# Optimization experiments

Measured on AMD Instinct MI355X. Metric: run time of the kernel, lower is better.

Reference implementation:

```python
import jax, jax.numpy as jnp
import numpy as np

N_NODES = 50000
N_EDGES = 800000
IN_FEATS = 128
OUT_FEATS = 128


def setup_inputs() -> dict:
    key = jax.random.key(0)
    k_feat, k_src, k_dst, k_w1, k_w2, k_lw = jax.random.split(key, 6)
    feat = jax.random.normal(k_feat, (N_NODES, IN_FEATS), dtype=jnp.float32)
    src_idx = jax.random.randint(k_src, (N_EDGES,), 0, N_NODES, dtype=jnp.int64 if jax.config.jax_enable_x64 else jnp.int32)
    dst_idx = jax.random.randint(k_dst, (N_EDGES,), 0, N_NODES, dtype=jnp.int64 if jax.config.jax_enable_x64 else jnp.int32)
    # xavier-uniform-ish scales
    w1_lim = float(np.sqrt(6.0 / (2 * IN_FEATS + IN_FEATS)))
    w2_lim = float(np.sqrt(6.0 / (IN_FEATS + OUT_FEATS)))
    lw_lim = float(np.sqrt(2.0) * np.sqrt(6.0 / (IN_FEATS + OUT_FEATS)))
    weight1 = jax.random.uniform(k_w1, (2 * IN_FEATS, IN_FEATS), jnp.float32, -w1_lim, w1_lim)
    weight2 = jax.random.uniform(k_w2, (IN_FEATS, OUT_FEATS), jnp.float32, -w2_lim, w2_lim)
    loop_weight = jax.random.uniform(k_lw, (IN_FEATS, OUT_FEATS), jnp.float32, -lw_lim, lw_lim)
    bias = jnp.zeros((OUT_FEATS,), dtype=jnp.float32)
    return {
        "feat": feat,
        "src_idx": src_idx,
        "dst_idx": dst_idx,
        "weight1": weight1,
        "weight2": weight2,
        "loop_weight": loop_weight,
        "bias": bias,
    }


def reference(feat, src_idx, dst_idx, weight1, weight2, loop_weight, bias):
    # Gather per-edge src/dst features and concat: [E, 2*d]
    feat_msg = jnp.concatenate([feat[src_idx], feat[dst_idx]], axis=-1)
    # 2-layer edge MLP: relu(msg @ W1) @ W2 -> [E, out]
    e_msg = jnp.matmul(jax.nn.relu(jnp.matmul(feat_msg, weight1)), weight2)
    # Scatter-sum to destination nodes: [N, out]
    rst = jax.ops.segment_sum(e_msg, dst_idx, num_segments=feat.shape[0])
    # bias + residual loop message
    rst = rst + bias + jnp.matmul(feat, loop_weight)
    return rst
```

## Files before the change

kernel.cpp:

```cpp
#include <hip/hip_runtime.h>

typedef __attribute__((ext_vector_type(8))) unsigned short ushort8v;
typedef __attribute__((ext_vector_type(8))) short short8v;
typedef __attribute__((ext_vector_type(4))) float f32x4;

#define CAP 64
#define BINSTRIDE 2560

__device__ inline unsigned short f2bf(float f) {
    union { float f; unsigned u; } v; v.f = f;
    unsigned u = v.u;
    unsigned r = (u + 0x7FFFu + ((u >> 16) & 1u)) >> 16;
    return (unsigned short)r;
}
__device__ inline float bf2f(unsigned short h) {
    union { unsigned u; float f; } v; v.u = ((unsigned)h) << 16;
    return v.f;
}
__device__ inline unsigned pkbf(float lo, float hi) {
    unsigned r;
    asm("v_cvt_pk_bf16_f32 %0, %1, %2" : "=v"(r) : "v"(lo), "v"(hi));
    return r;
}

__global__ __launch_bounds__(256) void prep_weights(
    const float* __restrict__ W1, const float* __restrict__ W2,
    const float* __restrict__ LW,
    unsigned short* __restrict__ W1t, unsigned short* __restrict__ W3t,
    int* __restrict__ binCur, int NBINS) {
    int tid = threadIdx.x;
    if (blockIdx.x == 0)
        for (int j = tid; j < NBINS; j += 256) binCur[j] = 0;
    int i = blockIdx.x * 256 + tid;
    if (i < 32768) {
        int jj = i >> 7, k = i & 127;
        float v = (jj < 128) ? W1[k * 128 + jj] : W1[(128 + k) * 128 + (jj - 128)];
        W1t[i] = f2bf(v);
    } else {
        int i2 = i - 32768;
        int n = i2 >> 8, k = i2 & 255;
        float v = (k < 128) ? W2[k * 128 + n] : LW[(k - 128) * 128 + n];
        W3t[i2] = f2bf(v);
    }
}

__global__ __launch_bounds__(256) void gemm1_bin(
    const float* __restrict__ feat, const unsigned short* __restrict__ W1t,
    unsigned short* __restrict__ AB,
    const int* __restrict__ src, const int* __restrict__ dst,
    int* __restrict__ binCur, unsigned* __restrict__ binPairs,
    int E, int NC, int NT, int M, int NBINS) {
    __shared__ unsigned short smem[(128 + 256) * 64];
    const int tid = threadIdx.x;
    const int bid = blockIdx.x;

    if ((bid & 1) == 0) {
        int tile = bid >> 1;
        if (tile >= NT) return;
        int m0 = tile * 128;
        const int lane = tid & 63, w = tid >> 6;
        const int wr = w >> 1, wc = w & 1;
        const int q = lane >> 4, ln = lane & 15;
        unsigned short* As = smem;
        unsigned short* Bs = smem + 128 * 64;

        f32x4 acc[4][8];
#pragma unroll
        for (int i = 0; i < 4; i++)
#pragma unroll
            for (int j = 0; j < 8; j++) acc[i][j] = (f32x4)0.f;

        for (int kk = 0; kk < 128; kk += 64) {
#pragma unroll
            for (int i = 0; i < 4; i++) {
                int id = i * 256 + tid;
                int r = id >> 3, bb = id & 7, gr = m0 + r;
                unsigned short* dstp = As + r * 64 + ((bb ^ (r & 7)) * 8);
                float4 lo = make_float4(0.f, 0.f, 0.f, 0.f), hi = lo;
                if (gr < M) {
                    const float* p = feat + (size_t)gr * 128 + kk + bb * 8;
                    lo = *(const float4*)p;
                    hi = *(const float4*)(p + 4);
                }
                *(uint4*)dstp = make_uint4(pkbf(lo.x, lo.y), pkbf(lo.z, lo.w),
                                           pkbf(hi.x, hi.y), pkbf(hi.z, hi.w));
            }
#pragma unroll
            for (int i = 0; i < 8; i++) {
                int id = i * 256 + tid;
                int r = id >> 3, bb = id & 7;
                ushort8v v = *(const ushort8v*)(W1t + (size_t)r * 128 + kk + bb * 8);
                *(ushort8v*)(Bs + r * 64 + ((bb ^ (r & 7)) * 8)) = v;
            }
            __syncthreads();
#pragma unroll
            for (int ks = 0; ks < 2; ks++) {
                short8v af[4], bv[8];
#pragma unroll
                for (int ti = 0; ti < 4; ti++) {
                    int m = wr * 64 + ti * 16 + ln;
                    int blk = (ks * 4 + q) ^ (m & 7);
                    af[ti] = *(const short8v*)(As + m * 64 + blk * 8);
                }
#pragma unroll
                for (int tj = 0; tj < 8; tj++) {
                    int n = wc * 128 + tj * 16 + ln;
                    int blk = (ks * 4 + q) ^ (n & 7);
                    bv[tj] = *(const short8v*)(Bs + n * 64 + blk * 8);
                }
#pragma unroll
                for (int ti = 0; ti < 4; ti++)
#pragma unroll
                    for (int tj = 0; tj < 8; tj++)
                        acc[ti][tj] = __builtin_amdgcn_mfma_f32_16x16x32_bf16(
                            af[ti], bv[tj], acc[ti][tj], 0, 0, 0);
            }
            if (kk == 0) __syncthreads();
        }
#pragma unroll
        for (int ti = 0; ti < 4; ti++) {
            int rowb = m0 + wr * 64 + ti * 16 + q * 4;
#pragma unroll
            for (int tj = 0; tj < 8; tj++) {
                int col = wc * 128 + tj * 16 + ln;
                f32x4 c = acc[ti][tj];
#pragma unroll
                for (int r = 0; r < 4; r++) {
                    int row = rowb + r;
                    if (row < M)
                        AB[(size_t)row * 256 + col] = f2bf(c[r]);
                }
            }
        }
    } else {
        int chunk = bid >> 1;
        if (chunk >= NC) return;
        int* hist = (int*)smem;
        int* bse = hist + 512;
        for (int j = tid; j < NBINS; j += 256) hist[j] = 0;

        int s[8], d[8];
        int base = chunk * 2048 + tid * 8;
        if (base + 7 < E) {
            int4 s0 = *(const int4*)(src + base);
            int4 s1 = *(const int4*)(src + base + 4);
            int4 d0 = *(const int4*)(dst + base);
            int4 d1 = *(const int4*)(dst + base + 4);
            s[0] = s0.x; s[1] = s0.y; s[2] = s0.z; s[3] = s0.w;
            s[4] = s1.x; s[5] = s1.y; s[6] = s1.z; s[7] = s1.w;
            d[0] = d0.x; d[1] = d0.y; d[2] = d0.z; d[3] = d0.w;
            d[4] = d1.x; d[5] = d1.y; d[6] = d1.z; d[7] = d1.w;
        } else {
#pragma unroll
            for (int k = 0; k < 8; k++) {
                int ee = base + k;
                if (ee < E) { d[k] = dst[ee]; s[k] = src[ee]; }
                else d[k] = -1;
            }
        }
        __syncthreads();
#pragma unroll
        for (int k = 0; k < 8; k++)
            if (d[k] >= 0) atomicAdd(&hist[d[k] >> 7], 1);
        __syncthreads();
        for (int j = tid; j < NBINS; j += 256) {
            int c = hist[j];
            bse[j] = c ? atomicAdd(&binCur[j], c) : 0;
            hist[j] = 0;
        }
        __syncthreads();
#pragma unroll
        for (int k = 0; k < 8; k++) {
            if (d[k] < 0) continue;
            int b = d[k] >> 7;
            int p = bse[b] + atomicAdd(&hist[b], 1);
            if (p < BINSTRIDE)
                binPairs[(size_t)b * BINSTRIDE + p] =
                    ((unsigned)(d[k] & 127) << 16) | (unsigned)s[k];
        }
    }
}

__global__ __launch_bounds__(256) void build_buckets(
    const int* __restrict__ binCur, const unsigned* __restrict__ binPairs,
    int* __restrict__ cur, unsigned short* __restrict__ eSrc,
    int N, int NBINS) {
    __shared__ unsigned pairs[BINSTRIDE];
    __shared__ int deg[128], rnk[128];
    int b = blockIdx.x, tid = threadIdx.x;
    if (b >= NBINS) return;
    int cnt = min(binCur[b], BINSTRIDE);
    if (tid < 128) { deg[tid] = 0; rnk[tid] = 0; }
    __syncthreads();
    for (int i = tid; i < cnt; i += 256) {
        unsigned pr = binPairs[(size_t)b * BINSTRIDE + i];
        pairs[i] = pr;
        atomicAdd(&deg[pr >> 16], 1);
    }
    __syncthreads();
    int node0 = b << 7;
    if (tid < 128 && node0 + tid < N) cur[node0 + tid] = deg[tid];
    for (int i = tid; i < cnt; i += 256) {
        unsigned pr = pairs[i];
        int dl = pr >> 16;
        int pos = atomicAdd(&rnk[dl], 1);
        if (pos < CAP)
            eSrc[(size_t)(node0 + dl) * CAP + pos] = (unsigned short)(pr & 0xFFFF);
    }
}

template <int BK, int AMODE, bool OUT_BF16>
__device__ void gemm_tile(
    unsigned short* As, unsigned short* Bs,
    const unsigned short* __restrict__ Abf, int lda,
    const float* __restrict__ Af32,
    const unsigned short* __restrict__ Bt, int ldb, int nRowsB,
    void* __restrict__ Cout, int ldc,
    const float* __restrict__ bias, int M, int K, int m0, int n0) {
    const int tid = threadIdx.x;
    const int lane = tid & 63;
    const int w = tid >> 6;
    const int wr = w >> 1, wc = w & 1;
    const int q = lane >> 4, ln = lane & 15;
    const int BPR = BK / 8;
    const int ITERS = BK / 16;

    f32x4 acc[4][4];
#pragma unroll
    for (int i = 0; i < 4; i++)
#pragma unroll
        for (int j = 0; j < 4; j++) acc[i][j] = (f32x4)0.f;

    for (int kk = 0; kk < K; kk += BK) {
        const bool aF32 = (AMODE == 1) || (AMODE == 2 && kk >= 128);
#pragma unroll
        for (int i = 0; i < ITERS; i++) {
            int id = i * 256 + tid;
            int r = id / BPR, bb = id % BPR;
            int gr = m0 + r;
            unsigned short* dstp = As + r * BK + ((bb ^ (r & (BPR - 1))) * 8);
            if (aF32) {
                float4 lo = make_float4(0.f, 0.f, 0.f, 0.f), hi = lo;
                if (gr < M) {
                    const float* p = Af32 + (size_t)gr * 128 +
                                     (AMODE == 2 ? kk - 128 : kk) + bb * 8;
                    lo = *(const float4*)p;
                    hi = *(const float4*)(p + 4);
                }
                *(uint4*)dstp = make_uint4(pkbf(lo.x, lo.y), pkbf(lo.z, lo.w),
                                           pkbf(hi.x, hi.y), pkbf(hi.z, hi.w));
            } else {
                ushort8v v = (ushort8v)(unsigned short)0;
                if (gr < M) v = *(const ushort8v*)(Abf + (size_t)gr * lda + kk + bb * 8);
                *(ushort8v*)dstp = v;
            }
        }
#pragma unroll
        for (int i = 0; i < ITERS; i++) {
            int id = i * 256 + tid;
            int r = id / BPR, bb = id % BPR;
            ushort8v v = (ushort8v)(unsigned short)0;
            int gr = n0 + r;
            if (gr < nRowsB) v = *(const ushort8v*)(Bt + (size_t)gr * ldb + kk + bb * 8);
            *(ushort8v*)(Bs + r * BK + ((bb ^ (r & (BPR - 1))) * 8)) = v;
        }
        __syncthreads();
#pragma unroll
        for (int ks = 0; ks < BK / 32; ks++) {
            short8v af[4], bfv[4];
#pragma unroll
            for (int ti = 0; ti < 4; ti++) {
                int m = wr * 64 + ti * 16 + ln;
                int blk = (ks * 4 + q) ^ (m & (BPR - 1));
                af[ti] = *(const short8v*)(As + m * BK + blk * 8);
            }
#pragma unroll
            for (int tj = 0; tj < 4; tj++) {
                int n = wc * 64 + tj * 16 + ln;
                int blk = (ks * 4 + q) ^ (n & (BPR - 1));
                bfv[tj] = *(const short8v*)(Bs + n * BK + blk * 8);
            }
#pragma unroll
            for (int ti = 0; ti < 4; ti++)
#pragma unroll
                for (int tj = 0; tj < 4; tj++)
                    acc[ti][tj] = __builtin_amdgcn_mfma_f32_16x16x32_bf16(
                        af[ti], bfv[tj], acc[ti][tj], 0, 0, 0);
        }
        if (kk + BK < K) __syncthreads();
    }

#pragma unroll
    for (int ti = 0; ti < 4; ti++) {
        int rowb = m0 + wr * 64 + ti * 16 + q * 4;
#pragma unroll
        for (int tj = 0; tj < 4; tj++) {
            int col = n0 + wc * 64 + tj * 16 + ln;
            f32x4 c = acc[ti][tj];
            float bv = 0.f;
            if (!OUT_BF16 && bias) bv = bias[col];
#pragma unroll
            for (int r = 0; r < 4; r++) {
                int row = rowb + r;
                if (row < M) {
                    if (OUT_BF16)
                        ((unsigned short*)Cout)[(size_t)row * ldc + col] = f2bf(c[r]);
                    else
                        ((float*)Cout)[(size_t)row * ldc + col] = c[r] + bv;
                }
            }
        }
    }
}

__global__ __launch_bounds__(256) void gemm2_kernel(
    const unsigned short* __restrict__ S2, const float* __restrict__ feat,
    const unsigned short* __restrict__ W3t,
    float* __restrict__ out, const float* __restrict__ bias, int M) {
    __shared__ unsigned short smem[2 * 128 * 64];
    gemm_tile<64, 2, false>(smem, smem + 128 * 64, S2, 128, feat, W3t, 256, 128,
                            (void*)out, 128, bias, M, 256, blockIdx.x * 128, 0);
}

__global__ __launch_bounds__(256) void gather_kernel(
    const unsigned short* __restrict__ AB, const int* __restrict__ cur,
    const unsigned short* __restrict__ eSrc,
    unsigned short* __restrict__ S2, int N) {
    int wid = (blockIdx.x * 256 + threadIdx.x) >> 6;
    int lane = threadIdx.x & 63;
    if (wid >= N) return;
    int num = min(cur[wid], CAP);
    size_t start = (size_t)wid * CAP;
    int half = lane >> 5, ln32 = lane & 31;
    ushort4 bv = *(const ushort4*)(AB + (size_t)wid * 256 + 128 + ln32 * 4);
    float b0 = bf2f(bv.x), b1 = bf2f(bv.y), b2 = bf2f(bv.z), b3 = bf2f(bv.w);
    float p0 = 0.f, p1 = 0.f, p2 = 0.f, p3 = 0.f;

    int mySrc = (lane < num) ? (int)eSrc[start + lane] : 0;
    int j = 0;
    for (; j + 16 <= num; j += 16) {
        ushort4 v[8];
#pragma unroll
        for (int u = 0; u < 8; u++) {
            int s = __shfl(mySrc, j + 2 * u + half);
            v[u] = *(const ushort4*)(AB + (size_t)s * 256 + ln32 * 4);
        }
#pragma unroll
        for (int u = 0; u < 8; u++) {
            p0 += fmaxf(bf2f(v[u].x) + b0, 0.f);
            p1 += fmaxf(bf2f(v[u].y) + b1, 0.f);
            p2 += fmaxf(bf2f(v[u].z) + b2, 0.f);
            p3 += fmaxf(bf2f(v[u].w) + b3, 0.f);
        }
    }
    for (; j + 4 <= num; j += 4) {
        ushort4 v[2];
#pragma unroll
        for (int u = 0; u < 2; u++) {
            int s = __shfl(mySrc, j + 2 * u + half);
            v[u] = *(const ushort4*)(AB + (size_t)s * 256 + ln32 * 4);
        }
#pragma unroll
        for (int u = 0; u < 2; u++) {
            p0 += fmaxf(bf2f(v[u].x) + b0, 0.f);
            p1 += fmaxf(bf2f(v[u].y) + b1, 0.f);
            p2 += fmaxf(bf2f(v[u].z) + b2, 0.f);
            p3 += fmaxf(bf2f(v[u].w) + b3, 0.f);
        }
    }
    for (; j < num; j += 2) {
        int idx = j + half;
        int s = __shfl(mySrc, idx);
        bool ok = idx < num;
        ushort4 v = *(const ushort4*)(AB + (size_t)s * 256 + ln32 * 4);
        float m = ok ? 1.f : 0.f;
        p0 += m * fmaxf(bf2f(v.x) + b0, 0.f);
        p1 += m * fmaxf(bf2f(v.y) + b1, 0.f);
        p2 += m * fmaxf(bf2f(v.z) + b2, 0.f);
        p3 += m * fmaxf(bf2f(v.w) + b3, 0.f);
    }
    p0 += __shfl_xor(p0, 32);
    p1 += __shfl_xor(p1, 32);
    p2 += __shfl_xor(p2, 32);
    p3 += __shfl_xor(p3, 32);
    if (half == 0) {
        *(ushort4*)(S2 + (size_t)wid * 128 + ln32 * 4) =
            make_ushort4(f2bf(p0), f2bf(p1), f2bf(p2), f2bf(p3));
    }
}

extern "C" void kernel_launch(void* const* d_in, const int* in_sizes, int n_in,
                              void* d_out, int out_size, void* d_ws, size_t ws_size,
                              hipStream_t stream) {
    const float* feat = (const float*)d_in[0];
    const int* src = (const int*)d_in[1];
    const int* dst = (const int*)d_in[2];
    const float* W1 = (const float*)d_in[3];
    const float* W2 = (const float*)d_in[4];
    const float* LW = (const float*)d_in[5];
    const float* bias = (const float*)d_in[6];
    float* out = (float*)d_out;

    const int N = in_sizes[0] / 128;
    const int E = in_sizes[1];
    const int NBINS = (N + 127) / 128;

    char* ws = (char*)d_ws;
    unsigned short* S2 = (unsigned short*)ws;
    size_t off = (size_t)N * 128 * 2;
    unsigned short* AB = (unsigned short*)(ws + off);
    off += (size_t)N * 256 * 2;
    unsigned short* W1t = (unsigned short*)(ws + off);
    off += (size_t)256 * 128 * 2;
    unsigned short* W3t = (unsigned short*)(ws + off);
    off += (size_t)128 * 256 * 2;
    int* cur = (int*)(ws + off);
    off += (size_t)N * 4;
    unsigned short* eSrc = (unsigned short*)(ws + off);
    off += (size_t)N * CAP * 2;
    int* binCur = (int*)(ws + off);
    off += (size_t)NBINS * 4;
    unsigned* binPairs = (unsigned*)(ws + off);
    off += (size_t)NBINS * BINSTRIDE * 4;

    prep_weights<<<256, 256, 0, stream>>>(W1, W2, LW, W1t, W3t, binCur, NBINS);

    int NT = (N + 127) / 128;
    int NC = (E + 2047) / 2048;
    int mx = NT > NC ? NT : NC;
    gemm1_bin<<<2 * mx, 256, 0, stream>>>(
        feat, W1t, AB, src, dst, binCur, binPairs, E, NC, NT, N, NBINS);

    build_buckets<<<NBINS, 256, 0, stream>>>(binCur, binPairs, cur, eSrc, N, NBINS);

    gather_kernel<<<(N + 3) / 4, 256, 0, stream>>>(AB, cur, eSrc, S2, N);

    gemm2_kernel<<<(N + 127) / 128, 256, 0, stream>>>(S2, feat, W3t, out, bias, N);
}
```

Measured before the change: 182.1 us.

## Fuse gather into gemm2 via LDS staging and split gemm1 into N-halves

The per-node gather-reduce now runs inside the second GEMM kernel. Each block aggregates 128 nodes into a swizzled LDS A-tile, then multiplies by the combined W2/loop weights, so the S2 intermediate no longer makes a round trip through global memory and one launch is dropped. gemm1 now computes 128x128 output tiles instead of 128x256, which halves its accumulator registers and LDS footprint and improves occupancy. Binning chunks grow to 4096 edges, and gemm and binning blocks are interleaved 4:1. The risk is that the fused kernel has only about 391 blocks, each doing a long serial gather with heavy 64KB LDS use, so latency hiding may suffer relative to the previous wave-per-node gather.

```diff
diff --git a/kernel.cpp b/kernel.cpp
--- a/kernel.cpp
+++ b/kernel.cpp
@@ -49,26 +49,27 @@
     unsigned short* __restrict__ AB,
     const int* __restrict__ src, const int* __restrict__ dst,
     int* __restrict__ binCur, unsigned* __restrict__ binPairs,
-    int E, int NC, int NT, int M, int NBINS) {
-    __shared__ unsigned short smem[(128 + 256) * 64];
+    int E, int NC, int NT2, int M, int NBINS) {
+    __shared__ unsigned short smem[2 * 128 * 64];
     const int tid = threadIdx.x;
     const int bid = blockIdx.x;
-
-    if ((bid & 1) == 0) {
-        int tile = bid >> 1;
-        if (tile >= NT) return;
-        int m0 = tile * 128;
+    const int r5 = bid % 5;
+
+    if (r5 < 4) {
+        int g = (bid / 5) * 4 + r5;
+        if (g >= NT2) return;
+        int m0 = (g >> 1) * 128, n0 = (g & 1) * 128;
         const int lane = tid & 63, w = tid >> 6;
         const int wr = w >> 1, wc = w & 1;
         const int q = lane >> 4, ln = lane & 15;
         unsigned short* As = smem;
         unsigned short* Bs = smem + 128 * 64;
 
-        f32x4 acc[4][8];
+        f32x4 acc[4][4];
 #pragma unroll
         for (int i = 0; i < 4; i++)
 #pragma unroll
-            for (int j = 0; j < 8; j++) acc[i][j] = (f32x4)0.f;
+            for (int j = 0; j < 4; j++) acc[i][j] = (f32x4)0.f;
 
         for (int kk = 0; kk < 128; kk += 64) {
 #pragma unroll
@@ -86,16 +87,16 @@
                                            pkbf(hi.x, hi.y), pkbf(hi.z, hi.w));
             }
 #pragma unroll
-            for (int i = 0; i < 8; i++) {
+            for (int i = 0; i < 4; i++) {
                 int id = i * 256 + tid;
                 int r = id >> 3, bb = id & 7;
-                ushort8v v = *(const ushort8v*)(W1t + (size_t)r * 128 + kk + bb * 8);
+                ushort8v v = *(const ushort8v*)(W1t + (size_t)(n0 + r) * 128 + kk + bb * 8);
                 *(ushort8v*)(Bs + r * 64 + ((bb ^ (r & 7)) * 8)) = v;
             }
             __syncthreads();
 #pragma unroll
             for (int ks = 0; ks < 2; ks++) {
-                short8v af[4], bv[8];
+                short8v af[4], bv[4];
 #pragma unroll
                 for (int ti = 0; ti < 4; ti++) {
                     int m = wr * 64 + ti * 16 + ln;
@@ -103,15 +104,15 @@
                     af[ti] = *(const short8v*)(As + m * 64 + blk * 8);
                 }
 #pragma unroll
-                for (int tj = 0; tj < 8; tj++) {
-                    int n = wc * 128 + tj * 16 + ln;
+                for (int tj = 0; tj < 4; tj++) {
+                    int n = wc * 64 + tj * 16 + ln;
                     int blk = (ks * 4 + q) ^ (n & 7);
                     bv[tj] = *(const short8v*)(Bs + n * 64 + blk * 8);
                 }
 #pragma unroll
                 for (int ti = 0; ti < 4; ti++)
 #pragma unroll
-                    for (int tj = 0; tj < 8; tj++)
+                    for (int tj = 0; tj < 4; tj++)
                         acc[ti][tj] = __builtin_amdgcn_mfma_f32_16x16x32_bf16(
                             af[ti], bv[tj], acc[ti][tj], 0, 0, 0);
             }
@@ -121,8 +122,8 @@
         for (int ti = 0; ti < 4; ti++) {
             int rowb = m0 + wr * 64 + ti * 16 + q * 4;
 #pragma unroll
-            for (int tj = 0; tj < 8; tj++) {
-                int col = wc * 128 + tj * 16 + ln;
+            for (int tj = 0; tj < 4; tj++) {
+                int col = n0 + wc * 64 + tj * 16 + ln;
                 f32x4 c = acc[ti][tj];
 #pragma unroll
                 for (int r = 0; r < 4; r++) {
@@ -133,34 +134,36 @@
             }
         }
     } else {
-        int chunk = bid >> 1;
+        int chunk = bid / 5;
         if (chunk >= NC) return;
         int* hist = (int*)smem;
         int* bse = hist + 512;
         for (int j = tid; j < NBINS; j += 256) hist[j] = 0;
 
-        int s[8], d[8];
-        int base = chunk * 2048 + tid * 8;
-        if (base + 7 < E) {
-            int4 s0 = *(const int4*)(src + base);
-            int4 s1 = *(const int4*)(src + base + 4);
-            int4 d0 = *(const int4*)(dst + base);
-            int4 d1 = *(const int4*)(dst + base + 4);
-            s[0] = s0.x; s[1] = s0.y; s[2] = s0.z; s[3] = s0.w;
-            s[4] = s1.x; s[5] = s1.y; s[6] = s1.z; s[7] = s1.w;
-            d[0] = d0.x; d[1] = d0.y; d[2] = d0.z; d[3] = d0.w;
-            d[4] = d1.x; d[5] = d1.y; d[6] = d1.z; d[7] = d1.w;
-        } else {
-#pragma unroll
-            for (int k = 0; k < 8; k++) {
-                int ee = base + k;
-                if (ee < E) { d[k] = dst[ee]; s[k] = src[ee]; }
-                else d[k] = -1;
+        int s[16], d[16];
+        int base = chunk * 4096;
+#pragma unroll
+        for (int i = 0; i < 4; i++) {
+            int e = base + i * 1024 + tid * 4;
+            if (e + 3 < E) {
+                int4 dv = *(const int4*)(dst + e);
+                int4 sv = *(const int4*)(src + e);
+                d[i * 4 + 0] = dv.x; d[i * 4 + 1] = dv.y;
+                d[i * 4 + 2] = dv.z; d[i * 4 + 3] = dv.w;
+                s[i * 4 + 0] = sv.x; s[i * 4 + 1] = sv.y;
+                s[i * 4 + 2] = sv.z; s[i * 4 + 3] = sv.w;
+            } else {
+#pragma unroll
+                for (int k = 0; k < 4; k++) {
+                    int ee = e + k;
+                    if (ee < E) { d[i * 4 + k] = dst[ee]; s[i * 4 + k] = src[ee]; }
+                    else d[i * 4 + k] = -1;
+                }
             }
         }
         __syncthreads();
 #pragma unroll
-        for (int k = 0; k < 8; k++)
+        for (int k = 0; k < 16; k++)
             if (d[k] >= 0) atomicAdd(&hist[d[k] >> 7], 1);
         __syncthreads();
         for (int j = tid; j < NBINS; j += 256) {
@@ -170,7 +173,7 @@
         }
         __syncthreads();
 #pragma unroll
-        for (int k = 0; k < 8; k++) {
+        for (int k = 0; k < 16; k++) {
             if (d[k] < 0) continue;
             int b = d[k] >> 7;
             int p = bse[b] + atomicAdd(&hist[b], 1);
@@ -209,85 +212,141 @@
     }
 }
 
-template <int BK, int AMODE, bool OUT_BF16>
-__device__ void gemm_tile(
-    unsigned short* As, unsigned short* Bs,
-    const unsigned short* __restrict__ Abf, int lda,
-    const float* __restrict__ Af32,
-    const unsigned short* __restrict__ Bt, int ldb, int nRowsB,
-    void* __restrict__ Cout, int ldc,
-    const float* __restrict__ bias, int M, int K, int m0, int n0) {
+__global__ __launch_bounds__(256) void gather_gemm2(
+    const unsigned short* __restrict__ AB, const int* __restrict__ cur,
+    const unsigned short* __restrict__ eSrc,
+    const float* __restrict__ feat, const unsigned short* __restrict__ W3t,
+    float* __restrict__ out, const float* __restrict__ bias, int M) {
+    __shared__ unsigned short As[128 * 128];
+    __shared__ unsigned short Bs[128 * 128];
     const int tid = threadIdx.x;
-    const int lane = tid & 63;
-    const int w = tid >> 6;
+    const int lane = tid & 63, w = tid >> 6;
+    const int m0 = blockIdx.x * 128;
+    const int half = lane >> 5, ln32 = lane & 31;
+
+    for (int i = 0; i < 32; i++) {
+        int r = w * 32 + i;
+        int wid = m0 + r;
+        int num = (wid < M) ? min(cur[wid], CAP) : 0;
+        size_t start = (size_t)wid * CAP;
+        float b0 = 0.f, b1 = 0.f, b2 = 0.f, b3 = 0.f;
+        if (wid < M) {
+            ushort4 bv = *(const ushort4*)(AB + (size_t)wid * 256 + 128 + ln32 * 4);
+            b0 = bf2f(bv.x); b1 = bf2f(bv.y); b2 = bf2f(bv.z); b3 = bf2f(bv.w);
+        }
+        float p0 = 0.f, p1 = 0.f, p2 = 0.f, p3 = 0.f;
+        int mySrc = (lane < num) ? (int)eSrc[start + lane] : 0;
+        int j = 0;
+        for (; j + 16 <= num; j += 16) {
+            ushort4 v[8];
+#pragma unroll
+            for (int u = 0; u < 8; u++) {
+                int s = __shfl(mySrc, j + 2 * u + half);
+                v[u] = *(const ushort4*)(AB + (size_t)s * 256 + ln32 * 4);
+            }
+#pragma unroll
+            for (int u = 0; u < 8; u++) {
+                p0 += fmaxf(bf2f(v[u].x) + b0, 0.f);
+                p1 += fmaxf(bf2f(v[u].y) + b1, 0.f);
+                p2 += fmaxf(bf2f(v[u].z) + b2, 0.f);
+                p3 += fmaxf(bf2f(v[u].w) + b3, 0.f);
+            }
+        }
+        for (; j + 4 <= num; j += 4) {
+            ushort4 v[2];
+#pragma unroll
+            for (int u = 0; u < 2; u++) {
+                int s = __shfl(mySrc, j + 2 * u + half);
+                v[u] = *(const ushort4*)(AB + (size_t)s * 256 + ln32 * 4);
+            }
+#pragma unroll
+            for (int u = 0; u < 2; u++) {
+                p0 += fmaxf(bf2f(v[u].x) + b0, 0.f);
+                p1 += fmaxf(bf2f(v[u].y) + b1, 0.f);
+                p2 += fmaxf(bf2f(v[u].z) + b2, 0.f);
+                p3 += fmaxf(bf2f(v[u].w) + b3, 0.f);
+            }
+        }
+        for (; j < num; j += 2) {
+            int idx = j + half;
+            int s = __shfl(mySrc, idx);
+            bool ok = idx < num;
+            ushort4 v = *(const ushort4*)(AB + (size_t)s * 256 + ln32 * 4);
+            float m = ok ? 1.f : 0.f;
+            p0 += m * fmaxf(bf2f(v.x) + b0, 0.f);
+            p1 += m * fmaxf(bf2f(v.y) + b1, 0.f);
+            p2 += m * fmaxf(bf2f(v.z) + b2, 0.f);
+            p3 += m * fmaxf(bf2f(v.w) + b3, 0.f);
+        }
+        p0 += __shfl_xor(p0, 32);
+        p1 += __shfl_xor(p1, 32);
+        p2 += __shfl_xor(p2, 32);
+        p3 += __shfl_xor(p3, 32);
+        if (half == 0) {
+            int bb = ln32 >> 1;
+            int off = ((bb ^ (r & 15)) * 8) + (ln32 & 1) * 4;
+            *(ushort4*)(As + r * 128 + off) =
+                make_ushort4(f2bf(p0), f2bf(p1), f2bf(p2), f2bf(p3));
+        }
+    }
+
     const int wr = w >> 1, wc = w & 1;
     const int q = lane >> 4, ln = lane & 15;
-    const int BPR = BK / 8;
-    const int ITERS = BK / 16;
-
     f32x4 acc[4][4];
 #pragma unroll
     for (int i = 0; i < 4; i++)
 #pragma unroll
         for (int j = 0; j < 4; j++) acc[i][j] = (f32x4)0.f;
 
-    for (int kk = 0; kk < K; kk += BK) {
-        const bool aF32 = (AMODE == 1) || (AMODE == 2 && kk >= 128);
-#pragma unroll
-        for (int i = 0; i < ITERS; i++) {
-            int id = i * 256 + tid;
-            int r = id / BPR, bb = id % BPR;
-            int gr = m0 + r;
-            unsigned short* dstp = As + r * BK + ((bb ^ (r & (BPR - 1))) * 8);
-            if (aF32) {
+#pragma unroll
+    for (int step = 0; step < 2; step++) {
+        if (step == 1) {
+#pragma unroll
+            for (int i = 0; i < 8; i++) {
+                int id = i * 256 + tid;
+                int r = id >> 4, bb = id & 15, gr = m0 + r;
+                unsigned short* dstp = As + r * 128 + ((bb ^ (r & 15)) * 8);
                 float4 lo = make_float4(0.f, 0.f, 0.f, 0.f), hi = lo;
                 if (gr < M) {
-                    const float* p = Af32 + (size_t)gr * 128 +
-                                     (AMODE == 2 ? kk - 128 : kk) + bb * 8;
+                    const float* p = feat + (size_t)gr * 128 + bb * 8;
                     lo = *(const float4*)p;
                     hi = *(const float4*)(p + 4);
                 }
                 *(uint4*)dstp = make_uint4(pkbf(lo.x, lo.y), pkbf(lo.z, lo.w),
                                            pkbf(hi.x, hi.y), pkbf(hi.z, hi.w));
-            } else {
-                ushort8v v = (ushort8v)(unsigned short)0;
-                if (gr < M) v = *(const ushort8v*)(Abf + (size_t)gr * lda + kk + bb * 8);
-                *(ushort8v*)dstp = v;
-            }
-        }
-#pragma unroll
-        for (int i = 0; i < ITERS; i++) {
+            }
+        }
+#pragma unroll
+        for (int i = 0; i < 8; i++) {
             int id = i * 256 + tid;
-            int r = id / BPR, bb = id % BPR;
-            ushort8v v = (ushort8v)(unsigned short)0;
-            int gr = n0 + r;
-            if (gr < nRowsB) v = *(const ushort8v*)(Bt + (size_t)gr * ldb + kk + bb * 8);
-            *(ushort8v*)(Bs + r * BK + ((bb ^ (r & (BPR - 1))) * 8)) = v;
+            int r = id >> 4, bb = id & 15;
+            ushort8v v = *(const ushort8v*)(W3t + (size_t)r * 256 + step * 128 + bb * 8);
+            *(ushort8v*)(Bs + r * 128 + ((bb ^ (r & 15)) * 8)) = v;
         }
         __syncthreads();
 #pragma unroll
-        for (int ks = 0; ks < BK / 32; ks++) {
-            short8v af[4], bfv[4];
+        for (int ks = 0; ks < 4; ks++) {
+            short8v af[4], bv[4];
 #pragma unroll
             for (int ti = 0; ti < 4; ti++) {
                 int m = wr * 64 + ti * 16 + ln;
-                int blk = (ks * 4 + q) ^ (m & (BPR - 1));
-                af[ti] = *(const short8v*)(As + m * BK + blk * 8);
+                int blk = (ks * 4 + q) ^ (m & 15);
+                af[ti] = *(const short8v*)(As + m * 128 + blk * 8);
             }
 #pragma unroll
             for (int tj = 0; tj < 4; tj++) {
                 int n = wc * 64 + tj * 16 + ln;
-                int blk = (ks * 4 + q) ^ (n & (BPR - 1));
-                bfv[tj] = *(const short8v*)(Bs + n * BK + blk * 8);
+                int blk = (ks * 4 + q) ^ (n & 15);
+                bv[tj] = *(const short8v*)(Bs + n * 128 + blk * 8);
             }
 #pragma unroll
             for (int ti = 0; ti < 4; ti++)
 #pragma unroll
                 for (int tj = 0; tj < 4; tj++)
                     acc[ti][tj] = __builtin_amdgcn_mfma_f32_16x16x32_bf16(
-                        af[ti], bfv[tj], acc[ti][tj], 0, 0, 0);
-        }
-        if (kk + BK < K) __syncthreads();
+                        af[ti], bv[tj], acc[ti][tj], 0, 0, 0);
+        }
+        if (step == 0) __syncthreads();
     }
 
 #pragma unroll
@@ -295,97 +354,16 @@
         int rowb = m0 + wr * 64 + ti * 16 + q * 4;
 #pragma unroll
         for (int tj = 0; tj < 4; tj++) {
-            int col = n0 + wc * 64 + tj * 16 + ln;
+            int col = wc * 64 + tj * 16 + ln;
             f32x4 c = acc[ti][tj];
-            float bv = 0.f;
-            if (!OUT_BF16 && bias) bv = bias[col];
+            float bv = bias[col];
 #pragma unroll
             for (int r = 0; r < 4; r++) {
                 int row = rowb + r;
-                if (row < M) {
-                    if (OUT_BF16)
-                        ((unsigned short*)Cout)[(size_t)row * ldc + col] = f2bf(c[r]);
-                    else
-                        ((float*)Cout)[(size_t)row * ldc + col] = c[r] + bv;
-                }
-            }
-        }
-    }
-}
-
-__global__ __launch_bounds__(256) void gemm2_kernel(
-    const unsigned short* __restrict__ S2, const float* __restrict__ feat,
-    const unsigned short* __restrict__ W3t,
-    float* __restrict__ out, const float* __restrict__ bias, int M) {
-    __shared__ unsigned short smem[2 * 128 * 64];
-    gemm_tile<64, 2, false>(smem, smem + 128 * 64, S2, 128, feat, W3t, 256, 128,
-                            (void*)out, 128, bias, M, 256, blockIdx.x * 128, 0);
-}
-
-__global__ __launch_bounds__(256) void gather_kernel(
-    const unsigned short* __restrict__ AB, const int* __restrict__ cur,
-    const unsigned short* __restrict__ eSrc,
-    unsigned short* __restrict__ S2, int N) {
-    int wid = (blockIdx.x * 256 + threadIdx.x) >> 6;
-    int lane = threadIdx.x & 63;
-    if (wid >= N) return;
-    int num = min(cur[wid], CAP);
-    size_t start = (size_t)wid * CAP;
-    int half = lane >> 5, ln32 = lane & 31;
-    ushort4 bv = *(const ushort4*)(AB + (size_t)wid * 256 + 128 + ln32 * 4);
-    float b0 = bf2f(bv.x), b1 = bf2f(bv.y), b2 = bf2f(bv.z), b3 = bf2f(bv.w);
-    float p0 = 0.f, p1 = 0.f, p2 = 0.f, p3 = 0.f;
-
-    int mySrc = (lane < num) ? (int)eSrc[start + lane] : 0;
-    int j = 0;
-    for (; j + 16 <= num; j += 16) {
-        ushort4 v[8];
-#pragma unroll
-        for (int u = 0; u < 8; u++) {
-            int s = __shfl(mySrc, j + 2 * u + half);
-            v[u] = *(const ushort4*)(AB + (size_t)s * 256 + ln32 * 4);
-        }
-#pragma unroll
-        for (int u = 0; u < 8; u++) {
-            p0 += fmaxf(bf2f(v[u].x) + b0, 0.f);
-            p1 += fmaxf(bf2f(v[u].y) + b1, 0.f);
-            p2 += fmaxf(bf2f(v[u].z) + b2, 0.f);
-            p3 += fmaxf(bf2f(v[u].w) + b3, 0.f);
-        }
-    }
-    for (; j + 4 <= num; j += 4) {
-        ushort4 v[2];
-#pragma unroll
-        for (int u = 0; u < 2; u++) {
-            int s = __shfl(mySrc, j + 2 * u + half);
-            v[u] = *(const ushort4*)(AB + (size_t)s * 256 + ln32 * 4);
-        }
-#pragma unroll
-        for (int u = 0; u < 2; u++) {
-            p0 += fmaxf(bf2f(v[u].x) + b0, 0.f);
-            p1 += fmaxf(bf2f(v[u].y) + b1, 0.f);
-            p2 += fmaxf(bf2f(v[u].z) + b2, 0.f);
-            p3 += fmaxf(bf2f(v[u].w) + b3, 0.f);
-        }
-    }
-    for (; j < num; j += 2) {
-        int idx = j + half;
-        int s = __shfl(mySrc, idx);
-        bool ok = idx < num;
-        ushort4 v = *(const ushort4*)(AB + (size_t)s * 256 + ln32 * 4);
-        float m = ok ? 1.f : 0.f;
-        p0 += m * fmaxf(bf2f(v.x) + b0, 0.f);
-        p1 += m * fmaxf(bf2f(v.y) + b1, 0.f);
-        p2 += m * fmaxf(bf2f(v.z) + b2, 0.f);
-        p3 += m * fmaxf(bf2f(v.w) + b3, 0.f);
-    }
-    p0 += __shfl_xor(p0, 32);
-    p1 += __shfl_xor(p1, 32);
-    p2 += __shfl_xor(p2, 32);
-    p3 += __shfl_xor(p3, 32);
-    if (half == 0) {
-        *(ushort4*)(S2 + (size_t)wid * 128 + ln32 * 4) =
-            make_ushort4(f2bf(p0), f2bf(p1), f2bf(p2), f2bf(p3));
+                if (row < M)
+                    out[(size_t)row * 128 + col] = c[r] + bv;
+            }
+        }
     }
 }
 
@@ -406,10 +384,8 @@
     const int NBINS = (N + 127) / 128;
 
     char* ws = (char*)d_ws;
-    unsigned short* S2 = (unsigned short*)ws;
-    size_t off = (size_t)N * 128 * 2;
-    unsigned short* AB = (unsigned short*)(ws + off);
-    off += (size_t)N * 256 * 2;
+    unsigned short* AB = (unsigned short*)ws;
+    size_t off = (size_t)N * 256 * 2;
     unsigned short* W1t = (unsigned short*)(ws + off);
     off += (size_t)256 * 128 * 2;
     unsigned short* W3t = (unsigned short*)(ws + off);
@@ -425,15 +401,15 @@
 
     prep_weights<<<256, 256, 0, stream>>>(W1, W2, LW, W1t, W3t, binCur, NBINS);
 
-    int NT = (N + 127) / 128;
-    int NC = (E + 2047) / 2048;
-    int mx = NT > NC ? NT : NC;
-    gemm1_bin<<<2 * mx, 256, 0, stream>>>(
-        feat, W1t, AB, src, dst, binCur, binPairs, E, NC, NT, N, NBINS);
+    int NT2 = ((N + 127) / 128) * 2;
+    int NC = (E + 4095) / 4096;
+    int NG = (NT2 + 3) / 4;
+    int mx = NG > NC ? NG : NC;
+    gemm1_bin<<<5 * mx, 256, 0, stream>>>(
+        feat, W1t, AB, src, dst, binCur, binPairs, E, NC, NT2, N, NBINS);
 
     build_buckets<<<NBINS, 256, 0, stream>>>(binCur, binPairs, cur, eSrc, N, NBINS);
 
-    gather_kernel<<<(N + 3) / 4, 256, 0, stream>>>(AB, cur, eSrc, S2, N);
-
-    gemm2_kernel<<<(N + 127) / 128, 256, 0, stream>>>(S2, feat, W3t, out, bias, N);
-}
+    gather_gemm2<<<(N + 127) / 128, 256, 0, stream>>>(
+        AB, cur, eSrc, feat, W3t, out, bias, N);
+}
```

Result: slower. 206.2 us (+13.3%).
